# Performance work log

Measured on AMD Instinct MI355X. Metric: run time of the kernel, lower is better.

Reference implementation:

```python
import jax, jax.numpy as jnp
import numpy as np

H, E, DFF = 768, 8, 3072
B, S = 2, 1024


def setup_inputs() -> dict:
    key = jax.random.key(0)
    ks = jax.random.split(key, 4)
    scale = 1.0 / np.sqrt(H)
    return {
        "x": jax.random.normal(ks[0], (B, S, H), dtype=jnp.float32),
        "Wg": jax.random.normal(ks[1], (H, E), dtype=jnp.float32) * scale,
        "bg": jnp.zeros((E,), dtype=jnp.float32),
        "W1": jax.random.normal(ks[2], (E, H, DFF), dtype=jnp.float32) * scale,
        "b1": jnp.zeros((E, DFF), dtype=jnp.float32),
        "W2": jax.random.normal(ks[3], (E, DFF, H), dtype=jnp.float32) * (1.0 / np.sqrt(DFF)),
        "b2": jnp.zeros((E, H), dtype=jnp.float32),
        "top_k": 2,
    }


def reference(x, Wg, bg, W1, b1, W2, b2, top_k):
    b, s, h = x.shape
    xf = x.reshape(-1, h)                       # [T, H]
    logits = xf @ Wg + bg                        # [T, E]
    probs = jax.nn.softmax(logits, axis=-1)
    w, idx = jax.lax.top_k(probs, top_k)         # [T, K]
    w = w / jnp.sum(w, axis=-1, keepdims=True)   # renormalize top-k weights
    # dense combine weights per (token, expert): [T, E]
    comb = jnp.sum(jax.nn.one_hot(idx, W1.shape[0], dtype=xf.dtype) * w[..., None], axis=1)
    # per-expert MLP: Linear -> exact GELU -> Linear
    hmid = jax.nn.gelu(jnp.einsum('th,ehf->etf', xf, W1) + b1[:, None, :], approximate=False)
    eo = jnp.einsum('etf,efh->eth', hmid, W2) + b2[:, None, :]   # [E, T, H]
    out = jnp.einsum('te,eth->th', comb, eo)     # weighted combine
    return out.reshape(b, s, h)
```

## Files before the change

### kernel.cpp

```cpp
#include <hip/hip_runtime.h>
#include <hip/hip_bf16.h>
#include <math.h>

#define H_DIM 768
#define E_NUM 8
#define DFF   3072
#define T_NUM 2048
#define PAIRS 4096

typedef __attribute__((ext_vector_type(8))) short          s16x8;
typedef __attribute__((ext_vector_type(4))) float          f32x4;
typedef __attribute__((ext_vector_type(4))) unsigned int   u32x4;
typedef __attribute__((ext_vector_type(4))) unsigned short u16x4;
typedef __attribute__((ext_vector_type(8))) unsigned short u16x8;

__device__ __forceinline__ unsigned short f2bf(float f) {
  unsigned int u = __builtin_bit_cast(unsigned int, f);
  u += 0x7FFFu + ((u >> 16) & 1u);
  return (unsigned short)(u >> 16);
}

__device__ __forceinline__ float bf2f(unsigned short v) {
  unsigned int u = ((unsigned int)v) << 16;
  return __builtin_bit_cast(float, u);
}

__device__ __forceinline__ float gelu_fast(float x) {
  float t = x * x;
  float a = __builtin_fmaf(t, -0.10294221f, -2.3022082f);
  float w;
  asm("v_exp_f32 %0, %1" : "=v"(w) : "v"(x * a));
  float r;
  float d = 1.0f + w;
  asm("v_rcp_f32 %0, %1" : "=v"(r) : "v"(d));
  return x * r;
}

__global__ __launch_bounds__(256) void k_route(
    const float* __restrict__ x, const float* __restrict__ Wg,
    const float* __restrict__ bg, int* __restrict__ eidx, float* __restrict__ ew) {
  int wave = threadIdx.x >> 6, lane = threadIdx.x & 63;
  int t = blockIdx.x * 4 + wave;
  const float* xr = x + (size_t)t * H_DIM;
  float acc[E_NUM];
#pragma unroll
  for (int e = 0; e < E_NUM; ++e) acc[e] = 0.f;
#pragma unroll
  for (int i = 0; i < H_DIM / 64; ++i) {
    int h = i * 64 + lane;
    float xv = xr[h];
    f32x4 w0 = *(const f32x4*)&Wg[h * 8];
    f32x4 w1 = *(const f32x4*)&Wg[h * 8 + 4];
    acc[0] += xv * w0[0]; acc[1] += xv * w0[1];
    acc[2] += xv * w0[2]; acc[3] += xv * w0[3];
    acc[4] += xv * w1[0]; acc[5] += xv * w1[1];
    acc[6] += xv * w1[2]; acc[7] += xv * w1[3];
  }
#pragma unroll
  for (int e = 0; e < E_NUM; ++e) {
#pragma unroll
    for (int off = 32; off > 0; off >>= 1) acc[e] += __shfl_xor(acc[e], off);
  }
  if (lane == 0) {
    float l[E_NUM];
#pragma unroll
    for (int e = 0; e < E_NUM; ++e) l[e] = acc[e] + bg[e];
    int i0 = 0;
#pragma unroll
    for (int e = 1; e < E_NUM; ++e) if (l[e] > l[i0]) i0 = e;
    int i1 = (i0 == 0) ? 1 : 0;
#pragma unroll
    for (int e = 0; e < E_NUM; ++e) if (e != i0 && l[e] > l[i1]) i1 = e;
    float d  = expf(l[i1] - l[i0]);
    eidx[2 * t]     = i0;
    eidx[2 * t + 1] = i1;
    ew[2 * t]       = 1.f / (1.f + d);
    ew[2 * t + 1]   = d / (1.f + d);
  }
}

__global__ __launch_bounds__(256) void k_build(
    const int* __restrict__ eidx, int* __restrict__ counts, int* __restrict__ offsets,
    int* __restrict__ tok_of, int* __restrict__ slot_of) {
  __shared__ int cnt[E_NUM];
  __shared__ int cur[E_NUM];
  int tid = threadIdx.x;
  if (tid < E_NUM) cnt[tid] = 0;
  __syncthreads();
#pragma unroll
  for (int i = 0; i < PAIRS / 256; ++i)
    atomicAdd(&cnt[eidx[i * 256 + tid]], 1);
  __syncthreads();
  if (tid == 0) {
    int s = 0;
    for (int e = 0; e < E_NUM; ++e) { cur[e] = s; s += cnt[e]; }
  }
  __syncthreads();
  if (tid < E_NUM) { counts[tid] = cnt[tid]; offsets[tid] = cur[tid]; }
#pragma unroll
  for (int i = 0; i < PAIRS / 256; ++i) {
    int p = i * 256 + tid;
    int s = atomicAdd(&cur[eidx[p]], 1);
    tok_of[s] = p >> 1;
    slot_of[p] = s;
  }
}

__global__ void k_gather(const float* __restrict__ x, const int* __restrict__ tok_of,
                         unsigned short* __restrict__ Xg) {
  int s = blockIdx.x;
  int lane = threadIdx.x;
  int t = tok_of[s];
  const f32x4* xr = (const f32x4*)(x + (size_t)t * H_DIM);
  u16x4* orow = (u16x4*)(Xg + (size_t)s * H_DIM);
#pragma unroll
  for (int i = 0; i < H_DIM / 256; ++i) {
    f32x4 v = xr[i * 64 + lane];
    u16x4 o;
    o[0] = f2bf(v[0]); o[1] = f2bf(v[1]); o[2] = f2bf(v[2]); o[3] = f2bf(v[3]);
    orow[i * 64 + lane] = o;
  }
}

__global__ __launch_bounds__(256) void k_transpose_cast(
    const float* __restrict__ in, unsigned short* __restrict__ out, int R, int C) {
  __shared__ unsigned short tile[64][72];
  int e  = blockIdx.z;
  int c0 = blockIdx.x * 64, r0 = blockIdx.y * 64;
  const float* ip = in + (size_t)e * R * C;
  unsigned short* op = out + (size_t)e * R * C;
  int tid = threadIdx.x;
  int tx = tid & 15, ty = tid >> 4;
#pragma unroll
  for (int i = 0; i < 4; ++i) {
    int r = ty + 16 * i;
    f32x4 v = *(const f32x4*)&ip[(size_t)(r0 + r) * C + c0 + tx * 4];
    u16x4 o;
    o[0] = f2bf(v[0]); o[1] = f2bf(v[1]); o[2] = f2bf(v[2]); o[3] = f2bf(v[3]);
    *(u16x4*)&tile[r][tx * 4] = o;
  }
  __syncthreads();
  int c  = tid & 63;
  int rc = (tid >> 6) * 16;
#pragma unroll
  for (int h = 0; h < 2; ++h) {
    u16x8 o;
#pragma unroll
    for (int j = 0; j < 8; ++j) o[j] = tile[rc + h * 8 + j][c];
    *(u16x8*)&op[(size_t)(c0 + c) * R + r0 + rc + h * 8] = o;
  }
}

template <int KTOT, int NT, int NSPLIT, int MT_MAX, bool GELU_OUT>
__global__ __launch_bounds__(512) void k_gemm(
    const unsigned short* __restrict__ A, const unsigned short* __restrict__ B,
    const float* __restrict__ bias, void* __restrict__ C,
    const int* __restrict__ counts, const int* __restrict__ offsets) {
  constexpr int NDIM  = NT * 128;
  constexpr int KLEN  = KTOT / NSPLIT;
  constexpr int NSTEP = KLEN / 64;
  int l = blockIdx.x;
  int nt = l % NT;  l /= NT;
  int e  = l & 7;   l >>= 3;
  int part = l % NSPLIT;
  int mt = l / NSPLIT;
  int Me = counts[e];
  if (mt * 256 >= Me) return;
  int seg = offsets[e];

  __shared__ __align__(16) unsigned short Al[2][256 * 64];
  __shared__ __align__(16) unsigned short Bl[2][128 * 64];

  int tid  = threadIdx.x;
  int lane = tid & 63;
  int wave = tid >> 6;
  int wm = wave >> 1, wn = wave & 1;

  int sr   = tid >> 3;
  int scl  = (tid & 7) * 8;
  int scs  = (((tid & 7) ^ (sr & 7)) * 8);
  int rxor = (lane & 7) << 3;

  f32x4 acc[4][4];
#pragma unroll
  for (int m = 0; m < 4; ++m)
#pragma unroll
    for (int n = 0; n < 4; ++n) acc[m][n] = (f32x4){0.f, 0.f, 0.f, 0.f};

  const unsigned short* Abase = A + (size_t)seg * KTOT;
  const unsigned short* Bbase = B + (size_t)e * NDIM * KTOT + (size_t)(nt * 128) * KTOT;
  const int kbeg = part * KLEN;

  auto stage = [&](int bb, int k0) {
#pragma unroll
    for (int j = 0; j < 4; ++j) {
      int row = j * 64 + sr;
      int r = mt * 256 + row;
      r = (r < Me) ? r : (Me - 1);
      const unsigned short* gp = Abase + (size_t)r * KTOT + k0 + scs;
      __builtin_amdgcn_global_load_lds(
          (__attribute__((address_space(1))) void*)gp,
          (__attribute__((address_space(3))) void*)&Al[bb][row * 64 + scl], 16, 0, 0);
    }
#pragma unroll
    for (int j = 0; j < 2; ++j) {
      int row = j * 64 + sr;
      const unsigned short* gp = Bbase + (size_t)row * KTOT + k0 + scs;
      __builtin_amdgcn_global_load_lds(
          (__attribute__((address_space(1))) void*)gp,
          (__attribute__((address_space(3))) void*)&Bl[bb][row * 64 + scl], 16, 0, 0);
    }
  };

  auto compute = [&](int bb) {
#pragma unroll
    for (int kk = 0; kk < 2; ++kk) {
      int ko = kk * 32 + (lane >> 4) * 8;
      s16x8 af[4], bfr[4];
#pragma unroll
      for (int m = 0; m < 4; ++m) {
        int row = wm * 64 + m * 16 + (lane & 15);
        u32x4 v = *(const u32x4*)&Al[bb][(row * 64 + ko) ^ rxor];
        af[m] = __builtin_bit_cast(s16x8, v);
      }
#pragma unroll
      for (int n = 0; n < 4; ++n) {
        int row = wn * 64 + n * 16 + (lane & 15);
        u32x4 v = *(const u32x4*)&Bl[bb][(row * 64 + ko) ^ rxor];
        bfr[n] = __builtin_bit_cast(s16x8, v);
      }
#pragma unroll
      for (int m = 0; m < 4; ++m)
#pragma unroll
        for (int n = 0; n < 4; ++n)
          acc[m][n] = __builtin_amdgcn_mfma_f32_16x16x32_bf16(af[m], bfr[n], acc[m][n], 0, 0, 0);
    }
  };

  stage(0, kbeg);
  stage(1, kbeg + 64);
  int cur = 0;
#pragma unroll
  for (int s = 0; s < NSTEP; ++s) {
    if (s + 1 < NSTEP) asm volatile("s_waitcnt vmcnt(6)" ::: "memory");
    else               asm volatile("s_waitcnt vmcnt(0)" ::: "memory");
    __builtin_amdgcn_s_barrier();
    compute(cur);
    if (s + 2 < NSTEP) {
      __builtin_amdgcn_s_barrier();
      stage(cur, kbeg + (s + 2) * 64);
    }
    cur ^= 1;
  }

  int rbase = mt * 256 + wm * 64;
  int cbase = nt * 128 + wn * 64;
#pragma unroll
  for (int m = 0; m < 4; ++m) {
#pragma unroll
    for (int n = 0; n < 4; ++n) {
      int col = cbase + n * 16 + (lane & 15);
      float bv = GELU_OUT ? bias[e * NDIM + col] : 0.f;
#pragma unroll
      for (int r = 0; r < 4; ++r) {
        int row = rbase + m * 16 + (lane >> 4) * 4 + r;
        if (row < Me) {
          float v = acc[m][n][r] + bv;
          size_t idx = ((size_t)part * PAIRS + seg + row) * NDIM + col;
          if constexpr (GELU_OUT) {
            ((unsigned short*)C)[idx] = f2bf(gelu_fast(v));
          } else {
            ((unsigned short*)C)[idx] = f2bf(v);
          }
        }
      }
    }
  }
}

template <int NSPLIT>
__global__ void k_combine(const unsigned short* __restrict__ P, const int* __restrict__ slot_of,
                          const int* __restrict__ eidx, const float* __restrict__ ew,
                          const float* __restrict__ b2, float* __restrict__ out) {
  int t = blockIdx.x;
  int i = threadIdx.x;
  int s0 = slot_of[2 * t], s1 = slot_of[2 * t + 1];
  int e0 = eidx[2 * t],    e1 = eidx[2 * t + 1];
  float w0 = ew[2 * t], w1 = ew[2 * t + 1];
  f32x4 a = *(const f32x4*)&b2[e0 * H_DIM + i * 4];
  f32x4 c = *(const f32x4*)&b2[e1 * H_DIM + i * 4];
#pragma unroll
  for (int p = 0; p < NSPLIT; ++p) {
    u16x4 va = *(const u16x4*)&P[((size_t)p * PAIRS + s0) * H_DIM + i * 4];
    u16x4 vb = *(const u16x4*)&P[((size_t)p * PAIRS + s1) * H_DIM + i * 4];
#pragma unroll
    for (int j = 0; j < 4; ++j) { a[j] += bf2f(va[j]); c[j] += bf2f(vb[j]); }
  }
  f32x4 o;
  o[0] = w0 * a[0] + w1 * c[0];
  o[1] = w0 * a[1] + w1 * c[1];
  o[2] = w0 * a[2] + w1 * c[2];
  o[3] = w0 * a[3] + w1 * c[3];
  ((f32x4*)(out + (size_t)t * H_DIM))[i] = o;
}

extern "C" void kernel_launch(void* const* d_in, const int* in_sizes, int n_in,
                              void* d_out, int out_size, void* d_ws, size_t ws_size,
                              hipStream_t stream) {
  (void)in_sizes; (void)n_in; (void)out_size;
  const float* x  = (const float*)d_in[0];
  const float* Wg = (const float*)d_in[1];
  const float* bg = (const float*)d_in[2];
  const float* W1 = (const float*)d_in[3];
  const float* b1 = (const float*)d_in[4];
  const float* W2 = (const float*)d_in[5];
  const float* b2 = (const float*)d_in[6];
  float* out = (float*)d_out;

  char* w = (char*)d_ws;
  size_t off = 0;
  auto take = [&](size_t n) { void* p = w + off; off = (off + n + 255) & ~(size_t)255; return p; };
  int*   ctrl    = (int*)  take(64 * sizeof(int));
  int*   eidx    = (int*)  take(PAIRS * sizeof(int));
  float* ew      = (float*)take(PAIRS * sizeof(float));
  int*   slot_of = (int*)  take(PAIRS * sizeof(int));
  int*   tok_of  = (int*)  take(PAIRS * sizeof(int));
  unsigned short* Xg   = (unsigned short*)take((size_t)PAIRS * H_DIM * 2);
  unsigned short* Wb   = (unsigned short*)take((size_t)E_NUM * H_DIM * DFF * 2);
  unsigned short* Hmid = (unsigned short*)take((size_t)PAIRS * DFF * 2);
  size_t p_off = off;
  unsigned short* P = (unsigned short*)(w + p_off);
  bool split4 = (p_off + (size_t)4 * PAIRS * H_DIM * 2) <= ws_size;
  if (p_off + (size_t)PAIRS * H_DIM * 2 > ws_size) return;

  int* counts  = ctrl;
  int* offsets = ctrl + 8;

  k_route<<<T_NUM / 4, 256, 0, stream>>>(x, Wg, bg, eidx, ew);
  k_build<<<1, 256, 0, stream>>>(eidx, counts, offsets, tok_of, slot_of);
  k_gather<<<PAIRS, 64, 0, stream>>>(x, tok_of, Xg);

  k_transpose_cast<<<dim3(DFF / 64, H_DIM / 64, E_NUM), 256, 0, stream>>>(W1, Wb, H_DIM, DFF);
  k_gemm<H_DIM, DFF / 128, 1, 4, true><<<(DFF / 128) * E_NUM * 4, 512, 0, stream>>>(
      Xg, Wb, b1, Hmid, counts, offsets);

  k_transpose_cast<<<dim3(H_DIM / 64, DFF / 64, E_NUM), 256, 0, stream>>>(W2, Wb, DFF, H_DIM);

  if (split4) {
    k_gemm<DFF, H_DIM / 128, 4, 4, false><<<(H_DIM / 128) * E_NUM * 4 * 4, 512, 0, stream>>>(
        Hmid, Wb, b2, P, counts, offsets);
    k_combine<4><<<T_NUM, 192, 0, stream>>>(P, slot_of, eidx, ew, b2, out);
  } else {
    k_gemm<DFF, H_DIM / 128, 1, 4, false><<<(H_DIM / 128) * E_NUM * 4, 512, 0, stream>>>(
        Hmid, Wb, b2, P, counts, offsets);
    k_combine<1><<<T_NUM, 192, 0, stream>>>(P, slot_of, eidx, ew, b2, out);
  }
}
```

Measured before the change: 169.5 us.

## Use 256x256 GEMM tiles with triple-buffered K=32 stages and XCD-aware expert mapping

Each GEMM block now computes a 256x256 tile, up from 256x128, with 8 waves in a 2x4 layout and 8x4 accumulators per wave. The K loop uses 32-wide slices in a three-deep LDS ring buffer instead of two 64-wide buffers. Blocks are remapped so experts rotate across XCDs, and the second GEMM now uses a 6-way K split. The aim is more operand reuse per LDS load, deeper prefetch, and better L2 locality per XCD. The cost is higher register pressure (launch bounds of 512 threads, 2 blocks), fewer blocks in the first GEMM, and more partial-sum traffic in the combine step. The fallback for a small workspace is removed.

```diff
diff --git a/kernel.cpp b/kernel.cpp
--- a/kernel.cpp
+++ b/kernel.cpp
@@ -152,111 +152,107 @@
 }
 
 template <int KTOT, int NT, int NSPLIT, int MT_MAX, bool GELU_OUT>
-__global__ __launch_bounds__(512) void k_gemm(
+__global__ __launch_bounds__(512, 2) void k_gemm(
     const unsigned short* __restrict__ A, const unsigned short* __restrict__ B,
     const float* __restrict__ bias, void* __restrict__ C,
     const int* __restrict__ counts, const int* __restrict__ offsets) {
-  constexpr int NDIM  = NT * 128;
+  constexpr int NDIM  = NT * 256;
   constexpr int KLEN  = KTOT / NSPLIT;
-  constexpr int NSTEP = KLEN / 64;
-  int l = blockIdx.x;
-  int nt = l % NT;  l /= NT;
-  int e  = l & 7;   l >>= 3;
-  int part = l % NSPLIT;
-  int mt = l / NSPLIT;
+  constexpr int NSTEP = KLEN / 32;
+  int b   = blockIdx.x;
+  int xcd = b & 7;
+  int i   = b >> 3;
+  int mt  = i % MT_MAX;
+  int g   = i / MT_MAX;
+  int e   = (g + xcd) & 7;
+  int nt  = g % NT;
+  int part = g / NT;
   int Me = counts[e];
   if (mt * 256 >= Me) return;
   int seg = offsets[e];
 
-  __shared__ __align__(16) unsigned short Al[2][256 * 64];
-  __shared__ __align__(16) unsigned short Bl[2][128 * 64];
+  __shared__ __align__(16) unsigned short Al[3][256 * 32];
+  __shared__ __align__(16) unsigned short Bl[3][256 * 32];
 
   int tid  = threadIdx.x;
   int lane = tid & 63;
   int wave = tid >> 6;
-  int wm = wave >> 1, wn = wave & 1;
-
-  int sr   = tid >> 3;
-  int scl  = (tid & 7) * 8;
-  int scs  = (((tid & 7) ^ (sr & 7)) * 8);
-  int rxor = (lane & 7) << 3;
-
-  f32x4 acc[4][4];
-#pragma unroll
-  for (int m = 0; m < 4; ++m)
+  int wm = wave >> 2, wn = wave & 3;
+
+  int sr   = tid >> 2;
+  int scl  = (tid & 3) * 8;
+  int scs  = (((tid & 3) ^ (sr & 3)) * 8);
+  int rxor = (lane & 3) << 3;
+
+  f32x4 acc[8][4];
+#pragma unroll
+  for (int m = 0; m < 8; ++m)
 #pragma unroll
     for (int n = 0; n < 4; ++n) acc[m][n] = (f32x4){0.f, 0.f, 0.f, 0.f};
 
   const unsigned short* Abase = A + (size_t)seg * KTOT;
-  const unsigned short* Bbase = B + (size_t)e * NDIM * KTOT + (size_t)(nt * 128) * KTOT;
+  const unsigned short* Bbase = B + (size_t)e * NDIM * KTOT + (size_t)(nt * 256) * KTOT;
   const int kbeg = part * KLEN;
 
   auto stage = [&](int bb, int k0) {
 #pragma unroll
-    for (int j = 0; j < 4; ++j) {
-      int row = j * 64 + sr;
+    for (int j = 0; j < 2; ++j) {
+      int row = j * 128 + sr;
       int r = mt * 256 + row;
       r = (r < Me) ? r : (Me - 1);
       const unsigned short* gp = Abase + (size_t)r * KTOT + k0 + scs;
       __builtin_amdgcn_global_load_lds(
           (__attribute__((address_space(1))) void*)gp,
-          (__attribute__((address_space(3))) void*)&Al[bb][row * 64 + scl], 16, 0, 0);
+          (__attribute__((address_space(3))) void*)&Al[bb][row * 32 + scl], 16, 0, 0);
     }
 #pragma unroll
     for (int j = 0; j < 2; ++j) {
-      int row = j * 64 + sr;
+      int row = j * 128 + sr;
       const unsigned short* gp = Bbase + (size_t)row * KTOT + k0 + scs;
       __builtin_amdgcn_global_load_lds(
           (__attribute__((address_space(1))) void*)gp,
-          (__attribute__((address_space(3))) void*)&Bl[bb][row * 64 + scl], 16, 0, 0);
+          (__attribute__((address_space(3))) void*)&Bl[bb][row * 32 + scl], 16, 0, 0);
     }
   };
 
   auto compute = [&](int bb) {
-#pragma unroll
-    for (int kk = 0; kk < 2; ++kk) {
-      int ko = kk * 32 + (lane >> 4) * 8;
-      s16x8 af[4], bfr[4];
-#pragma unroll
-      for (int m = 0; m < 4; ++m) {
-        int row = wm * 64 + m * 16 + (lane & 15);
-        u32x4 v = *(const u32x4*)&Al[bb][(row * 64 + ko) ^ rxor];
-        af[m] = __builtin_bit_cast(s16x8, v);
-      }
-#pragma unroll
-      for (int n = 0; n < 4; ++n) {
-        int row = wn * 64 + n * 16 + (lane & 15);
-        u32x4 v = *(const u32x4*)&Bl[bb][(row * 64 + ko) ^ rxor];
-        bfr[n] = __builtin_bit_cast(s16x8, v);
-      }
-#pragma unroll
-      for (int m = 0; m < 4; ++m)
-#pragma unroll
-        for (int n = 0; n < 4; ++n)
-          acc[m][n] = __builtin_amdgcn_mfma_f32_16x16x32_bf16(af[m], bfr[n], acc[m][n], 0, 0, 0);
+    int ko = (lane >> 4) * 8;
+    s16x8 bfr[4];
+#pragma unroll
+    for (int n = 0; n < 4; ++n) {
+      int row = wn * 64 + n * 16 + (lane & 15);
+      u32x4 v = *(const u32x4*)&Bl[bb][(row * 32 + ko) ^ rxor];
+      bfr[n] = __builtin_bit_cast(s16x8, v);
+    }
+#pragma unroll
+    for (int m = 0; m < 8; ++m) {
+      int row = wm * 128 + m * 16 + (lane & 15);
+      u32x4 v = *(const u32x4*)&Al[bb][(row * 32 + ko) ^ rxor];
+      s16x8 af = __builtin_bit_cast(s16x8, v);
+#pragma unroll
+      for (int n = 0; n < 4; ++n)
+        acc[m][n] = __builtin_amdgcn_mfma_f32_16x16x32_bf16(af, bfr[n], acc[m][n], 0, 0, 0);
     }
   };
 
   stage(0, kbeg);
-  stage(1, kbeg + 64);
-  int cur = 0;
+  stage(1, kbeg + 32);
+  stage(2, kbeg + 64);
 #pragma unroll
   for (int s = 0; s < NSTEP; ++s) {
-    if (s + 1 < NSTEP) asm volatile("s_waitcnt vmcnt(6)" ::: "memory");
-    else               asm volatile("s_waitcnt vmcnt(0)" ::: "memory");
+    if (s + 2 < NSTEP)      asm volatile("s_waitcnt vmcnt(8)" ::: "memory");
+    else if (s + 1 < NSTEP) asm volatile("s_waitcnt vmcnt(4)" ::: "memory");
+    else                    asm volatile("s_waitcnt vmcnt(0)" ::: "memory");
     __builtin_amdgcn_s_barrier();
-    compute(cur);
-    if (s + 2 < NSTEP) {
-      __builtin_amdgcn_s_barrier();
-      stage(cur, kbeg + (s + 2) * 64);
-    }
-    cur ^= 1;
-  }
-
-  int rbase = mt * 256 + wm * 64;
-  int cbase = nt * 128 + wn * 64;
-#pragma unroll
-  for (int m = 0; m < 4; ++m) {
+    compute(s % 3);
+    __builtin_amdgcn_s_barrier();
+    if (s + 3 < NSTEP) stage(s % 3, kbeg + (s + 3) * 32);
+  }
+
+  int rbase = mt * 256 + wm * 128;
+  int cbase = nt * 256 + wn * 64;
+#pragma unroll
+  for (int m = 0; m < 8; ++m) {
 #pragma unroll
     for (int n = 0; n < 4; ++n) {
       int col = cbase + n * 16 + (lane & 15);
@@ -328,10 +324,8 @@
   unsigned short* Xg   = (unsigned short*)take((size_t)PAIRS * H_DIM * 2);
   unsigned short* Wb   = (unsigned short*)take((size_t)E_NUM * H_DIM * DFF * 2);
   unsigned short* Hmid = (unsigned short*)take((size_t)PAIRS * DFF * 2);
-  size_t p_off = off;
-  unsigned short* P = (unsigned short*)(w + p_off);
-  bool split4 = (p_off + (size_t)4 * PAIRS * H_DIM * 2) <= ws_size;
-  if (p_off + (size_t)PAIRS * H_DIM * 2 > ws_size) return;
+  unsigned short* P    = (unsigned short*)take((size_t)6 * PAIRS * H_DIM * 2);
+  if (off > ws_size) return;
 
   int* counts  = ctrl;
   int* offsets = ctrl + 8;
@@ -341,18 +335,12 @@
   k_gather<<<PAIRS, 64, 0, stream>>>(x, tok_of, Xg);
 
   k_transpose_cast<<<dim3(DFF / 64, H_DIM / 64, E_NUM), 256, 0, stream>>>(W1, Wb, H_DIM, DFF);
-  k_gemm<H_DIM, DFF / 128, 1, 4, true><<<(DFF / 128) * E_NUM * 4, 512, 0, stream>>>(
+  k_gemm<H_DIM, DFF / 256, 1, 4, true><<<8 * (DFF / 256) * 4, 512, 0, stream>>>(
       Xg, Wb, b1, Hmid, counts, offsets);
 
   k_transpose_cast<<<dim3(H_DIM / 64, DFF / 64, E_NUM), 256, 0, stream>>>(W2, Wb, DFF, H_DIM);
 
-  if (split4) {
-    k_gemm<DFF, H_DIM / 128, 4, 4, false><<<(H_DIM / 128) * E_NUM * 4 * 4, 512, 0, stream>>>(
-        Hmid, Wb, b2, P, counts, offsets);
-    k_combine<4><<<T_NUM, 192, 0, stream>>>(P, slot_of, eidx, ew, b2, out);
-  } else {
-    k_gemm<DFF, H_DIM / 128, 1, 4, false><<<(H_DIM / 128) * E_NUM * 4, 512, 0, stream>>>(
-        Hmid, Wb, b2, P, counts, offsets);
-    k_combine<1><<<T_NUM, 192, 0, stream>>>(P, slot_of, eidx, ew, b2, out);
-  }
-}
+  k_gemm<DFF, H_DIM / 256, 6, 4, false><<<8 * (H_DIM / 256) * 6 * 4, 512, 0, stream>>>(
+      Hmid, Wb, b2, P, counts, offsets);
+  k_combine<6><<<T_NUM, 192, 0, stream>>>(P, slot_of, eidx, ew, b2, out);
+}
```

Measured after the change: 212.0 us. 1.25x slower.
